# Kernel tuning notes

Hardware: AMD Instinct MI355X
Metric: run time of the kernel (lower is better)

The kernel has to match this reference:

```python
import jax, jax.numpy as jnp
import numpy as np

N = 2048
H = W = 128


def setup_inputs() -> dict:
    key = jax.random.key(0)
    ks = jax.random.split(key, 8)
    # Gaussians placed in front of a pinhole camera at the origin (+z forward)
    xy = jax.random.normal(ks[0], (N, 2), dtype=jnp.float32) * 1.5
    z = jax.random.uniform(ks[1], (N, 1), dtype=jnp.float32, minval=2.0, maxval=6.0)
    mean = jnp.concatenate([xy, z], axis=-1)
    qvec = jax.random.normal(ks[2], (N, 4), dtype=jnp.float32)
    # raw scales -> exp activation gives scales around 0.05
    svec_raw = jax.random.normal(ks[3], (N, 3), dtype=jnp.float32) * 0.3 - 3.0
    color_raw = jax.random.normal(ks[4], (N, 3), dtype=jnp.float32)
    alpha_raw = jax.random.normal(ks[5], (N,), dtype=jnp.float32)
    bg = jax.random.uniform(ks[6], (3,), dtype=jnp.float32)
    viewmat = jnp.eye(4, dtype=jnp.float32)
    intrins = jnp.array([120.0, 120.0, W / 2.0, H / 2.0], dtype=jnp.float32)  # fx fy cx cy
    return dict(mean=mean, qvec=qvec, svec_raw=svec_raw, color_raw=color_raw,
                alpha_raw=alpha_raw, bg=bg, viewmat=viewmat, intrins=intrins)


def _quat_to_rotmat(q):
    q = q / jnp.linalg.norm(q, axis=-1, keepdims=True)
    w, x, y, z = q[..., 0], q[..., 1], q[..., 2], q[..., 3]
    R = jnp.stack([
        1 - 2 * (y * y + z * z), 2 * (x * y - w * z), 2 * (x * z + w * y),
        2 * (x * y + w * z), 1 - 2 * (x * x + z * z), 2 * (y * z - w * x),
        2 * (x * z - w * y), 2 * (y * z + w * x), 1 - 2 * (x * x + y * y),
    ], axis=-1)
    return R.reshape(q.shape[:-1] + (3, 3))


def reference(mean, qvec, svec_raw, color_raw, alpha_raw, bg, viewmat, intrins):
    fx, fy, cx, cy = intrins[0], intrins[1], intrins[2], intrins[3]
    # activations used by GaussianSplattingRenderer (svec_act=exp, alpha/color=sigmoid)
    svec = jnp.exp(svec_raw)
    alpha = jax.nn.sigmoid(alpha_raw)
    color = jax.nn.sigmoid(color_raw)

    Rw = viewmat[:3, :3]
    tw = viewmat[:3, 3]
    p_cam = mean @ Rw.T + tw                      # (N,3)
    x, y, z = p_cam[:, 0], p_cam[:, 1], p_cam[:, 2]
    zc = jnp.maximum(z, 1e-3)

    # 3D covariance Sigma = R diag(s)^2 R^T  via  M = R diag(s),  Sigma = M M^T
    Rq = _quat_to_rotmat(qvec)                    # (N,3,3)
    M = Rq * svec[:, None, :]                     # (N,3,3)

    # perspective Jacobian (EWA splatting), composed with view rotation
    zeros = jnp.zeros_like(zc)
    J = jnp.stack([
        jnp.stack([fx / zc, zeros, -fx * x / (zc * zc)], axis=-1),
        jnp.stack([zeros, fy / zc, -fy * y / (zc * zc)], axis=-1),
    ], axis=-2)                                   # (N,2,3)
    T = jnp.einsum('nij,jk->nik', J, Rw)          # (N,2,3)
    TM = jnp.einsum('nij,njk->nik', T, M)         # (N,2,3)
    cov2d = jnp.einsum('nij,nkj->nik', TM, TM)    # (N,2,2)
    cov2d = cov2d + 0.3 * jnp.eye(2, dtype=cov2d.dtype)  # low-pass filter

    a = cov2d[:, 0, 0]; b = cov2d[:, 0, 1]; c = cov2d[:, 1, 1]
    det = a * c - b * b
    det_safe = jnp.maximum(det, 1e-8)
    conic_a = c / det_safe; conic_b = -b / det_safe; conic_c = a / det_safe

    # projected 2D means
    u = fx * x / zc + cx
    v = fy * y / zc + cy

    px = jnp.arange(W, dtype=jnp.float32) + 0.5
    py = jnp.arange(H, dtype=jnp.float32) + 0.5
    dx = px[:, None] - u[None, :]                 # (W,N)
    dy = py[:, None] - v[None, :]                 # (H,N)

    power = (-0.5 * (conic_a * dx * dx)[None, :, :]
             - 0.5 * (conic_c * dy * dy)[:, None, :]
             - conic_b[None, None, :] * dx[None, :, :] * dy[:, None, :])  # (H,W,N)
    g = jnp.exp(jnp.minimum(power, 0.0))
    valid = (z > 0.2) & (det > 0)
    alpha_pix = jnp.where(valid[None, None, :], jnp.minimum(0.99, alpha * g), 0.0)

    # front-to-back depth order, sequential alpha compositing via cumprod
    order = jnp.argsort(z)
    alpha_s = alpha_pix[:, :, order]              # (H,W,N)
    color_s = color[order]                        # (N,3)
    Tcum = jnp.cumprod(1.0 - alpha_s, axis=-1)
    Tprev = jnp.concatenate([jnp.ones_like(Tcum[..., :1]), Tcum[..., :-1]], axis=-1)
    wgt = alpha_s * Tprev                         # (H,W,N)
    img = jnp.einsum('hwn,nc->hwc', wgt, color_s) + Tcum[..., -1:] * bg
    return img
```

## Files before the change

kernel.cpp:

```cpp
#include <hip/hip_runtime.h>
#include <math.h>

#define NG 2048
#define IMG_W 128
#define IMG_H 128
#define L2E 1.4426950408889634f
#define THR 18.0f
#define BLK 1024
#define NWAVE 16

typedef unsigned long long u64;

__device__ __forceinline__ float rlf(float x, int i) {
    return __int_as_float(__builtin_amdgcn_readlane(__float_as_int(x), i));
}

__device__ __forceinline__ float fexp2(float x) { return __builtin_amdgcn_exp2f(x); }
__device__ __forceinline__ float frcp(float x)  { return __builtin_amdgcn_rcpf(x); }
__device__ __forceinline__ float frsq(float x)  { return __builtin_amdgcn_rsqf(x); }
__device__ __forceinline__ float fsqr(float x)  { return __builtin_amdgcn_sqrtf(x); }
__device__ __forceinline__ float fexp(float x)  { return fexp2(x * L2E); }
__device__ __forceinline__ float fsig(float x)  { return frcp(1.f + fexp2(-x * L2E)); }

struct PrepOut {
    float u, v, A, B, C, al, cr, cg, cb, z, r2;
};

template <bool COLORS>
__device__ __forceinline__ PrepOut prep_g(
    int g,
    const float* __restrict__ mean, const float* __restrict__ qvec,
    const float* __restrict__ svec_raw, const float* __restrict__ color_raw,
    const float* __restrict__ alpha_raw,
    float fx, float fy, float cx, float cy,
    float R00, float R01, float R02, float t0,
    float R10, float R11, float R12, float t1,
    float R20, float R21, float R22, float t2)
{
    PrepOut o;
    float mx = mean[g * 3 + 0], my = mean[g * 3 + 1], mz = mean[g * 3 + 2];
    float x = R00 * mx + R01 * my + R02 * mz + t0;
    float y = R10 * mx + R11 * my + R12 * mz + t1;
    float z = R20 * mx + R21 * my + R22 * mz + t2;
    float zc = fmaxf(z, 0.001f);

    float qw = qvec[g * 4 + 0], qx = qvec[g * 4 + 1];
    float qy = qvec[g * 4 + 2], qz = qvec[g * 4 + 3];
    float qn = frsq(qw * qw + qx * qx + qy * qy + qz * qz);
    qw *= qn; qx *= qn; qy *= qn; qz *= qn;
    float Rq00 = 1.f - 2.f * (qy * qy + qz * qz), Rq01 = 2.f * (qx * qy - qw * qz), Rq02 = 2.f * (qx * qz + qw * qy);
    float Rq10 = 2.f * (qx * qy + qw * qz), Rq11 = 1.f - 2.f * (qx * qx + qz * qz), Rq12 = 2.f * (qy * qz - qw * qx);
    float Rq20 = 2.f * (qx * qz - qw * qy), Rq21 = 2.f * (qy * qz + qw * qx), Rq22 = 1.f - 2.f * (qx * qx + qy * qy);

    float s0 = fexp(svec_raw[g * 3 + 0]);
    float s1 = fexp(svec_raw[g * 3 + 1]);
    float s2 = fexp(svec_raw[g * 3 + 2]);
    float M00 = Rq00 * s0, M01 = Rq01 * s1, M02 = Rq02 * s2;
    float M10 = Rq10 * s0, M11 = Rq11 * s1, M12 = Rq12 * s2;
    float M20 = Rq20 * s0, M21 = Rq21 * s1, M22 = Rq22 * s2;

    float iz = frcp(zc);
    float J00 = fx * iz, J02 = -fx * x * iz * iz;
    float J11 = fy * iz, J12 = -fy * y * iz * iz;
    float T00 = J00 * R00 + J02 * R20;
    float T01 = J00 * R01 + J02 * R21;
    float T02 = J00 * R02 + J02 * R22;
    float T10 = J11 * R10 + J12 * R20;
    float T11 = J11 * R11 + J12 * R21;
    float T12 = J11 * R12 + J12 * R22;
    float TM00 = T00 * M00 + T01 * M10 + T02 * M20;
    float TM01 = T00 * M01 + T01 * M11 + T02 * M21;
    float TM02 = T00 * M02 + T01 * M12 + T02 * M22;
    float TM10 = T10 * M00 + T11 * M10 + T12 * M20;
    float TM11 = T10 * M01 + T11 * M11 + T12 * M21;
    float TM12 = T10 * M02 + T11 * M12 + T12 * M22;
    float a = TM00 * TM00 + TM01 * TM01 + TM02 * TM02 + 0.3f;
    float b = TM00 * TM10 + TM01 * TM11 + TM02 * TM12;
    float c = TM10 * TM10 + TM11 * TM11 + TM12 * TM12 + 0.3f;
    float det = a * c - b * b;
    float det_safe = fmaxf(det, 1e-8f);
    float inv_det = frcp(det_safe);
    bool valid = (z > 0.2f) && (det > 0.0f);

    float conic_a = c * inv_det;
    float conic_b = -b * inv_det;
    float conic_c = a * inv_det;

    float half_tr = 0.5f * (conic_a + conic_c);
    float half_df = 0.5f * (conic_a - conic_c);
    float lam_min = half_tr - fsqr(half_df * half_df + conic_b * conic_b);
    float r2 = (lam_min > 1e-20f) ? (1.05f * 2.0f * THR / (L2E * lam_min)) : 3.0e38f;
    if (!valid) r2 = -1.0f;

    o.u = fx * x * iz + cx;
    o.v = fy * y * iz + cy;
    o.A = -0.5f * L2E * conic_a;
    o.B = -L2E * conic_b;
    o.C = -0.5f * L2E * conic_c;
    o.z = z;
    o.r2 = r2;
    if (COLORS) {
        o.al = fsig(alpha_raw[g]);
        o.cr = fsig(color_raw[g * 3 + 0]);
        o.cg = fsig(color_raw[g * 3 + 1]);
        o.cb = fsig(color_raw[g * 3 + 2]);
    } else {
        o.al = o.cr = o.cg = o.cb = 0.f;
    }
    return o;
}

template <int NO>
__device__ __forceinline__ void sort_ranks(const u64* zkey,
                                           unsigned short* ssid,
                                           int K, int t)
{
    u64 myk[NO];
    int myr[NO];
#pragma unroll
    for (int o = 0; o < NO; ++o) {
        int j = t + BLK * o;
        myk[o] = (j < K) ? zkey[j] : ~0ull;
        myr[o] = 0;
    }
    const ulonglong2* z2 = (const ulonglong2*)zkey;
    const int np = (K + 1) >> 1;
    for (int i = 0; i < np; ++i) {
        ulonglong2 kk = z2[i];
#pragma unroll
        for (int o = 0; o < NO; ++o) {
            myr[o] += (kk.x < myk[o]) ? 1 : 0;
            myr[o] += (kk.y < myk[o]) ? 1 : 0;
        }
    }
#pragma unroll
    for (int o = 0; o < NO; ++o) {
        int j = t + BLK * o;
        if (j < K) ssid[myr[o]] = (unsigned short)(myk[o] & 0xFFFFu);
    }
}

__global__ __launch_bounds__(BLK) void splat_kernel(
    const float* __restrict__ mean, const float* __restrict__ qvec,
    const float* __restrict__ svec_raw, const float* __restrict__ color_raw,
    const float* __restrict__ alpha_raw, const float* __restrict__ bg,
    const float* __restrict__ viewmat, const float* __restrict__ intrins,
    float* __restrict__ out)
{
    __shared__ __align__(16) u64 zkey[NG + 2];
    __shared__ unsigned short ssid[NG];
    __shared__ float4 part[NWAVE][64];
    __shared__ int scnt;

    const int t = threadIdx.x;
    const int wave = t >> 6;
    const int lane = t & 63;
    const int tx = blockIdx.x, ty = blockIdx.y;

    if (t == 0) scnt = 0;

    const float fx = intrins[0], fy = intrins[1], cx = intrins[2], cy = intrins[3];
    const float R00 = viewmat[0], R01 = viewmat[1], R02 = viewmat[2],  t0 = viewmat[3];
    const float R10 = viewmat[4], R11 = viewmat[5], R12 = viewmat[6],  t1 = viewmat[7];
    const float R20 = viewmat[8], R21 = viewmat[9], R22 = viewmat[10], t2 = viewmat[11];

    const float x0 = tx * 8 + 0.5f, x1 = x0 + 7.0f;
    const float y0 = ty * 8 + 0.5f, y1 = y0 + 7.0f;

    __syncthreads();

#pragma unroll
    for (int k = 0; k < NG / BLK; ++k) {
        int g = k * BLK + t;
        PrepOut p = prep_g<false>(g, mean, qvec, svec_raw, color_raw,
                                  alpha_raw, fx, fy, cx, cy,
                                  R00, R01, R02, t0, R10, R11, R12, t1,
                                  R20, R21, R22, t2);
        float dxm = fmaxf(0.f, fmaxf(x0 - p.u, p.u - x1));
        float dym = fmaxf(0.f, fmaxf(y0 - p.v, p.v - y1));
        if (dxm * dxm + dym * dym <= p.r2) {
            int slot = atomicAdd(&scnt, 1);
            zkey[slot] = ((u64)__float_as_uint(p.z) << 16) | (unsigned)g;
        }
    }
    __syncthreads();
    const int K = scnt;
    if (t == 0) zkey[K] = ~0ull;
    __syncthreads();

    if (K > BLK) {
        sort_ranks<2>(zkey, ssid, K, t);
    } else if ((t & ~63) < K) {
        sort_ranks<1>(zkey, ssid, K, t);
    }
    __syncthreads();

    const float fpx = tx * 8 + (lane & 7) + 0.5f;
    const float fpy = ty * 8 + (lane >> 3) + 0.5f;
    float T = 1.f, Cr = 0.f, Cg = 0.f, Cb = 0.f;

    const int Kq = (K + NWAVE - 1) / NWAVE;
    const int s0 = wave * Kq;
    const int s1 = min(K, s0 + Kq);

    for (int base = s0; base < s1; base += 64) {
        const int j = base + lane;
        const bool inr = (j < s1);
        const int idx = inr ? (int)ssid[j] : 0;
        PrepOut p = prep_g<true>(idx, mean, qvec, svec_raw, color_raw,
                                 alpha_raw, fx, fy, cx, cy,
                                 R00, R01, R02, t0, R10, R11, R12, t1,
                                 R20, R21, R22, t2);
        u64 mask = __ballot(inr);
        while (mask) {
            const int i = (int)__builtin_ctzll(mask);
            mask &= mask - 1;
            float gu = rlf(p.u, i), gv_ = rlf(p.v, i);
            float gA = rlf(p.A, i), gB = rlf(p.B, i), gC = rlf(p.C, i);
            float al = rlf(p.al, i);
            float cr = rlf(p.cr, i), cg = rlf(p.cg, i), cb = rlf(p.cb, i);

            float dx = fpx - gu;
            float dy = fpy - gv_;
            float adx2 = gA * dx * dx;
            float bdx = gB * dx;
            float pw = fminf(fmaf(dy, fmaf(gC, dy, bdx), adx2), 0.f);
            float gv = fexp2(pw);
            float a = fminf(0.99f, al * gv);
            float w = a * T;
            Cr = fmaf(w, cr, Cr); Cg = fmaf(w, cg, Cg); Cb = fmaf(w, cb, Cb);
            T = fmaf(-a, T, T);
        }
        if (__all(T < 1e-6f)) break;
    }

    part[wave][lane] = make_float4(Cr, Cg, Cb, T);
    __syncthreads();

    if (wave == 0) {
        float4 acc = part[0][lane];
#pragma unroll
        for (int s = 1; s < NWAVE; ++s) {
            float4 p = part[s][lane];
            acc.x = fmaf(acc.w, p.x, acc.x);
            acc.y = fmaf(acc.w, p.y, acc.y);
            acc.z = fmaf(acc.w, p.z, acc.z);
            acc.w *= p.w;
        }
        const int col = tx * 8 + (lane & 7);
        const int row = ty * 8 + (lane >> 3);
        const int pix = row * IMG_W + col;
        out[pix * 3 + 0] = acc.x + acc.w * bg[0];
        out[pix * 3 + 1] = acc.y + acc.w * bg[1];
        out[pix * 3 + 2] = acc.z + acc.w * bg[2];
    }
}

extern "C" void kernel_launch(void* const* d_in, const int* in_sizes, int n_in,
                              void* d_out, int out_size, void* d_ws, size_t ws_size,
                              hipStream_t stream)
{
    const float* mean      = (const float*)d_in[0];
    const float* qvec      = (const float*)d_in[1];
    const float* svec_raw  = (const float*)d_in[2];
    const float* color_raw = (const float*)d_in[3];
    const float* alpha_raw = (const float*)d_in[4];
    const float* bg        = (const float*)d_in[5];
    const float* viewmat   = (const float*)d_in[6];
    const float* intrins   = (const float*)d_in[7];
    float* out = (float*)d_out;
    (void)d_ws; (void)ws_size;

    hipLaunchKernelGGL(splat_kernel, dim3(16, 16), dim3(BLK), 0, stream,
                       mean, qvec, svec_raw, color_raw, alpha_raw, bg,
                       viewmat, intrins, out);
}
```

Before: 75.18 us.

## Cache per-Gaussian projection records in LDS to avoid recomputing prep in raster loop

During the culling pass each surviving Gaussian's projected parameters, activated opacity and colors are written to a shared-memory record indexed by its slot. The sort now emits slot indices, and the raster loop reads the records from LDS instead of reloading inputs and recomputing the full projection and sigmoids per Gaussian. Slots beyond the record capacity fall back to recomputation. Colors are stored as packed fp16 to cut LDS footprint and readlane count, which lowers color precision slightly and raises shared-memory use, possibly affecting occupancy.

Result: no change. 75.67 us (+0.6%).

```diff
diff --git a/kernel.cpp b/kernel.cpp
--- a/kernel.cpp
+++ b/kernel.cpp
@@ -1,4 +1,5 @@
 #include <hip/hip_runtime.h>
+#include <hip/hip_fp16.h>
 #include <math.h>
 
 #define NG 2048
@@ -8,11 +9,15 @@
 #define THR 18.0f
 #define BLK 1024
 #define NWAVE 16
+#define RECMAX 1024
 
 typedef unsigned long long u64;
 
 __device__ __forceinline__ float rlf(float x, int i) {
     return __int_as_float(__builtin_amdgcn_readlane(__float_as_int(x), i));
+}
+__device__ __forceinline__ unsigned rlu(float x, int i) {
+    return (unsigned)__builtin_amdgcn_readlane(__float_as_int(x), i);
 }
 
 __device__ __forceinline__ float fexp2(float x) { return __builtin_amdgcn_exp2f(x); }
@@ -22,16 +27,19 @@
 __device__ __forceinline__ float fexp(float x)  { return fexp2(x * L2E); }
 __device__ __forceinline__ float fsig(float x)  { return frcp(1.f + fexp2(-x * L2E)); }
 
+__device__ __forceinline__ float pack2h(float a, float b) {
+    __half2 h = __floats2half2_rn(a, b);
+    return *reinterpret_cast<float*>(&h);
+}
+
 struct PrepOut {
-    float u, v, A, B, C, al, cr, cg, cb, z, r2;
+    float u, v, A, B, C, z, r2;
 };
 
-template <bool COLORS>
 __device__ __forceinline__ PrepOut prep_g(
     int g,
     const float* __restrict__ mean, const float* __restrict__ qvec,
-    const float* __restrict__ svec_raw, const float* __restrict__ color_raw,
-    const float* __restrict__ alpha_raw,
+    const float* __restrict__ svec_raw,
     float fx, float fy, float cx, float cy,
     float R00, float R01, float R02, float t0,
     float R10, float R11, float R12, float t1,
@@ -99,14 +107,6 @@
     o.C = -0.5f * L2E * conic_c;
     o.z = z;
     o.r2 = r2;
-    if (COLORS) {
-        o.al = fsig(alpha_raw[g]);
-        o.cr = fsig(color_raw[g * 3 + 0]);
-        o.cg = fsig(color_raw[g * 3 + 1]);
-        o.cb = fsig(color_raw[g * 3 + 2]);
-    } else {
-        o.al = o.cr = o.cg = o.cb = 0.f;
-    }
     return o;
 }
 
@@ -136,7 +136,7 @@
 #pragma unroll
     for (int o = 0; o < NO; ++o) {
         int j = t + BLK * o;
-        if (j < K) ssid[myr[o]] = (unsigned short)(myk[o] & 0xFFFFu);
+        if (j < K) ssid[myr[o]] = (unsigned short)j;
     }
 }
 
@@ -148,6 +148,7 @@
     float* __restrict__ out)
 {
     __shared__ __align__(16) u64 zkey[NG + 2];
+    __shared__ __align__(16) float4 rec[RECMAX * 2];
     __shared__ unsigned short ssid[NG];
     __shared__ float4 part[NWAVE][64];
     __shared__ int scnt;
@@ -172,15 +173,23 @@
 #pragma unroll
     for (int k = 0; k < NG / BLK; ++k) {
         int g = k * BLK + t;
-        PrepOut p = prep_g<false>(g, mean, qvec, svec_raw, color_raw,
-                                  alpha_raw, fx, fy, cx, cy,
-                                  R00, R01, R02, t0, R10, R11, R12, t1,
-                                  R20, R21, R22, t2);
+        PrepOut p = prep_g(g, mean, qvec, svec_raw, fx, fy, cx, cy,
+                           R00, R01, R02, t0, R10, R11, R12, t1,
+                           R20, R21, R22, t2);
         float dxm = fmaxf(0.f, fmaxf(x0 - p.u, p.u - x1));
         float dym = fmaxf(0.f, fmaxf(y0 - p.v, p.v - y1));
         if (dxm * dxm + dym * dym <= p.r2) {
             int slot = atomicAdd(&scnt, 1);
             zkey[slot] = ((u64)__float_as_uint(p.z) << 16) | (unsigned)g;
+            if (slot < RECMAX) {
+                float al = fsig(alpha_raw[g]);
+                float cr = fsig(color_raw[g * 3 + 0]);
+                float cg = fsig(color_raw[g * 3 + 1]);
+                float cb = fsig(color_raw[g * 3 + 2]);
+                rec[2 * slot + 0] = make_float4(p.u, p.v, p.A, p.B);
+                rec[2 * slot + 1] = make_float4(p.C, al, pack2h(cr, cg),
+                                                pack2h(cb, 0.f));
+            }
         }
     }
     __syncthreads();
@@ -206,19 +215,42 @@
     for (int base = s0; base < s1; base += 64) {
         const int j = base + lane;
         const bool inr = (j < s1);
-        const int idx = inr ? (int)ssid[j] : 0;
-        PrepOut p = prep_g<true>(idx, mean, qvec, svec_raw, color_raw,
-                                 alpha_raw, fx, fy, cx, cy,
-                                 R00, R01, R02, t0, R10, R11, R12, t1,
-                                 R20, R21, R22, t2);
+        const int slot = inr ? (int)ssid[j] : 0;
+        float4 r0, r1;
+        const bool spill = inr && (slot >= RECMAX);
+        if (__any(spill)) {
+            if (spill) {
+                int idx = (int)(zkey[slot] & 0xFFFFu);
+                PrepOut p = prep_g(idx, mean, qvec, svec_raw, fx, fy, cx, cy,
+                                   R00, R01, R02, t0, R10, R11, R12, t1,
+                                   R20, R21, R22, t2);
+                float al = fsig(alpha_raw[idx]);
+                float cr = fsig(color_raw[idx * 3 + 0]);
+                float cg = fsig(color_raw[idx * 3 + 1]);
+                float cb = fsig(color_raw[idx * 3 + 2]);
+                r0 = make_float4(p.u, p.v, p.A, p.B);
+                r1 = make_float4(p.C, al, pack2h(cr, cg), pack2h(cb, 0.f));
+            } else {
+                r0 = rec[2 * slot + 0];
+                r1 = rec[2 * slot + 1];
+            }
+        } else {
+            r0 = rec[2 * slot + 0];
+            r1 = rec[2 * slot + 1];
+        }
+
         u64 mask = __ballot(inr);
         while (mask) {
             const int i = (int)__builtin_ctzll(mask);
             mask &= mask - 1;
-            float gu = rlf(p.u, i), gv_ = rlf(p.v, i);
-            float gA = rlf(p.A, i), gB = rlf(p.B, i), gC = rlf(p.C, i);
-            float al = rlf(p.al, i);
-            float cr = rlf(p.cr, i), cg = rlf(p.cg, i), cb = rlf(p.cb, i);
+            float gu = rlf(r0.x, i), gv_ = rlf(r0.y, i);
+            float gA = rlf(r0.z, i), gB = rlf(r0.w, i);
+            float gC = rlf(r1.x, i), al = rlf(r1.y, i);
+            union { unsigned u; __half2 h; } urg; urg.u = rlu(r1.z, i);
+            union { unsigned u; __half2 h; } ubl; ubl.u = rlu(r1.w, i);
+            float cr = __half2float(__low2half(urg.h));
+            float cg = __half2float(__high2half(urg.h));
+            float cb = __half2float(__low2half(ubl.h));
 
             float dx = fpx - gu;
             float dy = fpy - gv_;
```
